# Kernel tuning notes

Hardware: AMD Instinct MI355X
Metric: run time of the kernel (lower is better)

## Reference

```python
import jax, jax.numpy as jnp
import numpy as np

MAX_DISP = 48
PATCH = 3
OFFSET = 0
PAD = PATCH // 2
EPS = 1e-3


def _unfold(x, P, pad):
    # x: [B,C,H,W] -> [B,C,K2,H,W], K2 enumerated row-major over the PxP window
    B, C, H, W = x.shape
    xp = jnp.pad(x, ((0, 0), (0, 0), (pad, pad), (pad, pad)))
    return jnp.stack([xp[:, :, i:i + H, j:j + W]
                      for i in range(P) for j in range(P)], axis=2)


def _normalize(x, axes):
    # torch F.normalize: x / clamp(||x||_2, min=eps)
    n = jnp.sqrt(jnp.sum(x * x, axis=axes, keepdims=True))
    return x / jnp.maximum(n, EPS)


def setup_inputs() -> dict:
    key = jax.random.key(0)
    k1, k2, k3 = jax.random.split(key, 3)
    shp = (2, 32, 128, 416)
    return {
        "xl": jax.random.normal(k1, shp, dtype=jnp.float32),
        "xm": jax.random.normal(k2, shp, dtype=jnp.float32),
        "xr": jax.random.normal(k3, shp, dtype=jnp.float32),
    }


def reference(xl, xm, xr):
    B, C, H, W = xl.shape
    K2 = PATCH * PATCH
    scale = (C * K2) ** 0.5

    pl = _normalize(_unfold(xl, PATCH, PAD), (1, 2))  # [B,C,K2,H,W]
    pr = _normalize(_unfold(xr, PATCH, PAD), (1, 2))
    fl = _normalize(xm, (1,))                          # [B,C,H,W]

    # fl is constant over the K2 axis, so sum patches over K2 once for sim_L/sim_R
    Sl = pl.sum(axis=2)  # [B,C,H,W]
    Sr = pr.sum(axis=2)

    cL, cR, cLR = [], [], []
    for d in range(OFFSET, OFFSET + MAX_DISP):
        if d > 0:
            # shifted_l[w] = patches_l[w+d] (zero right pad); shifted_r[w] = patches_r[w-d]
            sL = jnp.einsum('bchw,bchw->bhw', fl[..., :W - d], Sl[..., d:])
            sL = jnp.pad(sL, ((0, 0), (0, 0), (0, d)))
            sR = jnp.einsum('bchw,bchw->bhw', fl[..., d:], Sr[..., :W - d])
            sR = jnp.pad(sR, ((0, 0), (0, 0), (d, 0)))
            wlr = W - 2 * d  # overlap region of the two opposite shifts
            if wlr > 0:
                sLR = jnp.einsum('bckhw,bckhw->bhw', pl[..., 2 * d:], pr[..., :wlr])
                sLR = jnp.pad(sLR, ((0, 0), (0, 0), (d, d)))
            else:
                sLR = jnp.zeros((B, H, W), xl.dtype)
        else:
            sL = jnp.einsum('bchw,bchw->bhw', fl, Sl)
            sR = jnp.einsum('bchw,bchw->bhw', fl, Sr)
            sLR = jnp.einsum('bckhw,bckhw->bhw', pl, pr)
        cL.append(sL / scale)
        cR.append(sR / scale)
        cLR.append(sLR / scale)

    cost = jnp.stack([jnp.stack(cL, 1), jnp.stack(cR, 1), jnp.stack(cLR, 1)], axis=1)
    return jnp.clip(cost, -10.0, 10.0).astype(jnp.float16)  # [B,3,D,H,W]
```

## Files before the change

kernel.cpp:

```cpp
#include <hip/hip_runtime.h>
#include <math.h>

#define B 2
#define C 32
#define H 128
#define W 416
#define D 48
#define HW (H*W)
#define CHW (C*HW)
#define EPSN 1e-3f
#define ISCALE 0.05892556509887896f
#define LSTR 36
#define DSPL (D / 2)
#define DHALF (DSPL / 2)
#define SWZ(v) (((v) >> 1) & 7)

__device__ __forceinline__ float clip10(float x) {
    return fminf(fmaxf(x, -10.0f), 10.0f);
}

__global__ __launch_bounds__(256) void k_norm(const float* __restrict__ sql,
                                              const float* __restrict__ sqr,
                                              float* __restrict__ inl,
                                              float* __restrict__ inr) {
    int idx = blockIdx.x * 256 + threadIdx.x;
    if (idx >= B * HW) return;
    int b = idx / HW, hw = idx - b * HW;
    int h = hw / W, w = hw - h * W;
    float sl = 0.f, sr = 0.f;
#pragma unroll
    for (int di = -1; di <= 1; ++di) {
        int hh = h + di;
        if (hh < 0 || hh >= H) continue;
#pragma unroll
        for (int dj = -1; dj <= 1; ++dj) {
            int ww = w + dj;
            if (ww < 0 || ww >= W) continue;
            int p = b * HW + hh * W + ww;
            sl += sql[p];
            sr += sqr[p];
        }
    }
    inl[idx] = 1.0f / fmaxf(sqrtf(sl), EPSN);
    inr[idx] = 1.0f / fmaxf(sqrtf(sr), EPSN);
}

__device__ __forceinline__ void stage_row_v2(const float* __restrict__ gsrc,
                                             float* __restrict__ lds,
                                             int tid, int nthreads) {
    for (int t = tid; t < (W / 4) * C; t += nthreads) {
        int rw = t & 7;
        int cl = (t >> 3) & 7;
        int g  = t >> 6;
        int wg = g % 13;
        int ch = g / 13;
        int c  = ch * 8 + cl;
        int w4 = (wg * 8 + rw) * 4;
        float4 v = *(const float4*)(gsrc + (size_t)c * HW + w4);
        lds[(w4 + 0) * LSTR + c] = v.x;
        lds[(w4 + 1) * LSTR + c] = v.y;
        lds[(w4 + 2) * LSTR + c] = v.z;
        lds[(w4 + 3) * LSTR + c] = v.w;
    }
}

__device__ __forceinline__ void stage_row3_swz(const float* __restrict__ gsrc,
                                               float* __restrict__ lds,
                                               int h, int tid, int nthreads) {
    for (int t = tid; t < (W / 4) * C; t += nthreads) {
        int rw = t & 7;
        int cl = (t >> 3) & 7;
        int g  = t >> 6;
        int wg = g % 13;
        int ch = g / 13;
        int c  = ch * 8 + cl;
        int w4 = (wg * 8 + rw) * 4;
        const float* p = gsrc + (size_t)c * HW + w4;
        float4 v = *(const float4*)(p);
        if (h > 0) {
            float4 a = *(const float4*)(p - W);
            v.x += a.x; v.y += a.y; v.z += a.z; v.w += a.w;
        }
        if (h < H - 1) {
            float4 a = *(const float4*)(p + W);
            v.x += a.x; v.y += a.y; v.z += a.z; v.w += a.w;
        }
        int g2 = c >> 2, wd = c & 3;
        int sA = SWZ(w4);
        int sB_ = (sA + 1) & 7;
        lds[(w4 + 0) * LSTR + 4 * (g2 ^ sA) + wd] = v.x;
        lds[(w4 + 1) * LSTR + 4 * (g2 ^ sA) + wd] = v.y;
        lds[(w4 + 2) * LSTR + 4 * (g2 ^ sB_) + wd] = v.z;
        lds[(w4 + 3) * LSTR + 4 * (g2 ^ sB_) + wd] = v.w;
    }
}

__device__ __forceinline__ float dot32(const float* __restrict__ fl,
                                       const float* __restrict__ col) {
    const float4* c4 = (const float4*)col;
    float a = 0.0f;
#pragma unroll
    for (int q = 0; q < 8; ++q) {
        float4 v = c4[q];
        a += fl[4 * q + 0] * v.x + fl[4 * q + 1] * v.y
           + fl[4 * q + 2] * v.z + fl[4 * q + 3] * v.w;
    }
    return a;
}

__device__ __forceinline__ void dot32x2s(const float* __restrict__ fl0,
                                         const float* __restrict__ fl1,
                                         const float* __restrict__ col, int s,
                                         float& a0, float& a1) {
    const float4* c4 = (const float4*)col;
    float s0 = 0.f, s1 = 0.f;
#pragma unroll
    for (int q = 0; q < 8; ++q) {
        float4 v = c4[q ^ s];
        s0 += fl0[4 * q + 0] * v.x + fl0[4 * q + 1] * v.y
            + fl0[4 * q + 2] * v.z + fl0[4 * q + 3] * v.w;
        s1 += fl1[4 * q + 0] * v.x + fl1[4 * q + 1] * v.y
            + fl1[4 * q + 2] * v.z + fl1[4 * q + 3] * v.w;
    }
    a0 = s0; a1 = s1;
}

__global__ __launch_bounds__(448) void k_lr(const float* __restrict__ xm,
                                            const float* __restrict__ xl,
                                            const float* __restrict__ xr,
                                            const float* __restrict__ inl,
                                            const float* __restrict__ inr,
                                            float* __restrict__ out) {
    __shared__ float sB[W * LSTR];
    __shared__ float sIn[W];
    int tid = threadIdx.x;
    int h = blockIdx.x;
    int b = blockIdx.y;
    int d0 = blockIdx.z * DSPL;
    bool act = tid < W;
    int p = tid >> 1;
    int half = tid & 1;
    int w = 2 * p;
    int dbase = d0 + half * DHALF;
    int bhw = b * HW + h * W;
    const float* pm = xm + (size_t)b * CHW + h * W;

    float fl0[C], fl1[C];
    if (act) {
        float am0 = 0.f, am1 = 0.f;
#pragma unroll
        for (int c = 0; c < C; ++c) {
            float2 mv = *(const float2*)(pm + c * HW + w);
            fl0[c] = mv.x; fl1[c] = mv.y;
            am0 += mv.x * mv.x; am1 += mv.y * mv.y;
        }
        float im0 = 1.0f / fmaxf(sqrtf(am0), EPSN);
        float im1 = 1.0f / fmaxf(sqrtf(am1), EPSN);
#pragma unroll
        for (int c = 0; c < C; ++c) { fl0[c] *= im0; fl1[c] *= im1; }
    } else {
#pragma unroll
        for (int c = 0; c < C; ++c) { fl0[c] = 0.f; fl1[c] = 0.f; }
    }

    stage_row3_swz(xl + (size_t)b * CHW + h * W, sB, h, tid, 448);
    for (int j = tid; j < W; j += 448) sIn[j] = inl[bhw + j];
    __syncthreads();
    if (act) {
        float* o = out + ((size_t)b * 3 + 0) * D * HW + h * W;
        float g0a = 0.f, g0b = 0.f, g1a = 0.f, g1b = 0.f, s0p = 0.f;
#pragma unroll 3
        for (int j = 0; j <= DHALF + 2; ++j) {
            int v = w + dbase - 1 + j;
            float c0 = 0.f, c1 = 0.f;
            if (v >= 0 && v < W) dot32x2s(fl0, fl1, sB + v * LSTR, SWZ(v), c0, c1);
            float s0 = 0.f, s1 = 0.f;
            if (j >= 2) {
                int m = v - 1;
                if (m < W) {
                    float sc = sIn[m] * ISCALE;
                    s0 = clip10((g0a + g0b + c0) * sc);
                    s1 = clip10((g1a + g1b + c1) * sc);
                }
                if (j >= 3) {
                    int d = dbase + j - 3;
                    *(float2*)(o + (size_t)d * HW + w) = make_float2(s0p, s1);
                }
            }
            s0p = s0;
            g0a = g0b; g0b = c0;
            g1a = g1b; g1b = c1;
        }
    }
    __syncthreads();

    stage_row3_swz(xr + (size_t)b * CHW + h * W, sB, h, tid, 448);
    for (int j = tid; j < W; j += 448) sIn[j] = inr[bhw + j];
    __syncthreads();
    if (act) {
        float* o = out + ((size_t)b * 3 + 1) * D * HW + h * W;
        float g0a = 0.f, g0b = 0.f, g1a = 0.f, g1b = 0.f, s0p = 0.f;
#pragma unroll 3
        for (int j = 0; j <= DHALF + 2; ++j) {
            int v = w - dbase - DHALF + j;
            float c0 = 0.f, c1 = 0.f;
            if (v >= 0 && v < W) dot32x2s(fl0, fl1, sB + v * LSTR, SWZ(v), c0, c1);
            float s0 = 0.f, s1 = 0.f;
            if (j >= 2) {
                int m = v - 1;
                if (m >= 0) {
                    float sc = sIn[m] * ISCALE;
                    s0 = clip10((g0a + g0b + c0) * sc);
                    s1 = clip10((g1a + g1b + c1) * sc);
                }
                if (j >= 3) {
                    int d = dbase + DHALF + 2 - j;
                    *(float2*)(o + (size_t)d * HW + w) = make_float2(s0p, s1);
                }
            }
            s0p = s0;
            g0a = g0b; g0b = c0;
            g1a = g1b; g1b = c1;
        }
    }
}

__global__ __launch_bounds__(896) void k_e(const float* __restrict__ xl,
                                           const float* __restrict__ xr,
                                           float* __restrict__ EH,
                                           float* __restrict__ sql,
                                           float* __restrict__ sqr) {
    __shared__ float sXL[W * LSTR];
    int tid = threadIdx.x;
    int h = blockIdx.x;
    int b = blockIdx.y;
    int d0 = blockIdx.z * DSPL;
    int lane = tid & 63;
    int wv = tid >> 6;
    int half = (wv >= 7) ? 1 : 0;
    int wv7 = wv - 7 * half;
    int v = wv7 * 62 + lane - 1;
    bool vin = (v >= 0) && (v < W);
    const float* br = xr + (size_t)b * CHW + h * W;

    float xrv[C];
#pragma unroll
    for (int c = 0; c < C; ++c) xrv[c] = vin ? br[c * HW + v] : 0.0f;

    stage_row_v2(xl + (size_t)b * CHW + h * W, sXL, tid, 896);
    __syncthreads();

    bool wr = (lane >= 1) && (lane <= 62) && (v < W);

    if (blockIdx.z == 0 && half == 0) {
        float sr_ = 0.f, sl_ = 0.f;
#pragma unroll
        for (int c = 0; c < C; ++c) sr_ += xrv[c] * xrv[c];
        if (vin) {
            const float4* c4 = (const float4*)(sXL + v * LSTR);
#pragma unroll
            for (int q = 0; q < 8; ++q) {
                float4 x = c4[q];
                sl_ += x.x * x.x + x.y * x.y + x.z * x.z + x.w * x.w;
            }
        }
        if (wr) {
            sqr[b * HW + h * W + v] = sr_;
            sql[b * HW + h * W + v] = sl_;
        }
    }

    float* pe = EH + (((size_t)b * D) * H + h) * W + v;
    int dlo = d0 + half * DHALF;
    for (int d = dlo; d < dlo + DHALF; ++d) {
        int s = 2 * d;
        float e = 0.0f;
        if (vin && v + s < W) e = dot32(xrv, sXL + (v + s) * LSTR);
        float em = __shfl_up(e, 1);
        float ep = __shfl_down(e, 1);
        float eh = em + e + ep;
        if (wr) pe[(size_t)d * HW] = eh;
    }
}

#define DCH 12
__global__ __launch_bounds__(448) void k_lr2(const float* __restrict__ EH,
                                             const float* __restrict__ inl,
                                             const float* __restrict__ inr,
                                             float* __restrict__ out) {
    int w = threadIdx.x;
    int dc = blockIdx.x;
    int h = blockIdx.y;
    int b = blockIdx.z;
    if (w >= W) return;
    int bhw = b * HW + h * W;
    bool hm = (h > 0), hp = (h < H - 1);

    float* o = out + ((size_t)b * 3 + 2) * D * HW + h * W + w;
#pragma unroll
    for (int i = 0; i < DCH; ++i) {
        int d = dc * DCH + i;
        float r = 0.0f;
        if (w >= d && w + d < W) {
            int vc = w - d;
            const float* base = EH + ((size_t)b * D + d) * HW + vc;
            float e = base[h * W];
            if (hm) e += base[(h - 1) * W];
            if (hp) e += base[(h + 1) * W];
            float nl = inl[bhw + w + d];
            float nr = inr[bhw + vc];
            r = clip10(e * nl * nr * ISCALE);
        }
        o[(size_t)d * HW] = r;
    }
}

extern "C" void kernel_launch(void* const* d_in, const int* in_sizes, int n_in,
                              void* d_out, int out_size, void* d_ws, size_t ws_size,
                              hipStream_t stream) {
    const float* xl = (const float*)d_in[0];
    const float* xm = (const float*)d_in[1];
    const float* xr = (const float*)d_in[2];
    float* out = (float*)d_out;

    float* ws = (float*)d_ws;
    float* inl = ws;
    float* inr = inl + B * HW;
    float* sql = inr + B * HW;
    float* sqr = sql + B * HW;
    float* EH  = sqr + B * HW;

    k_e<<<dim3(H, B, 2), dim3(896), 0, stream>>>(xl, xr, EH, sql, sqr);
    k_norm<<<dim3((B * HW + 255) / 256), dim3(256), 0, stream>>>(sql, sqr, inl, inr);
    k_lr<<<dim3(H, B, 2), dim3(448), 0, stream>>>(xm, xl, xr, inl, inr, out);
    k_lr2<<<dim3(4, H, B), dim3(448), 0, stream>>>(EH, inl, inr, out);
}
```

Baseline: 183.1 us.

## Split k_lr over width chunks with windowed LDS staging; shrink k_e blocks

k_lr now splits each row into two width chunks of 208 columns and stages only the needed 240-column window of 3-row-summed features into LDS. This cuts shared memory per block and allows more resident blocks. Each thread pair now loads half of the xm channels and exchanges the rest via xor shuffles, and the LDS swizzle is recomputed relative to the window. k_e drops from 896 threads per block (each block covering both disparity halves) to 448 threads looping over all 24 disparities. That trades per-block parallelism for less duplicated xr loading and more blocks per CU.

```diff
diff --git a/kernel.cpp b/kernel.cpp
--- a/kernel.cpp
+++ b/kernel.cpp
@@ -13,7 +13,9 @@
 #define LSTR 36
 #define DSPL (D / 2)
 #define DHALF (DSPL / 2)
-#define SWZ(v) (((v) >> 1) & 7)
+#define WCH 208
+#define NQ 60
+#define NCOLA (NQ * 4)
 
 __device__ __forceinline__ float clip10(float x) {
     return fminf(fmaxf(x, -10.0f), 10.0f);
@@ -64,34 +66,50 @@
     }
 }
 
-__device__ __forceinline__ void stage_row3_swz(const float* __restrict__ gsrc,
-                                               float* __restrict__ lds,
-                                               int h, int tid, int nthreads) {
-    for (int t = tid; t < (W / 4) * C; t += nthreads) {
-        int rw = t & 7;
-        int cl = (t >> 3) & 7;
-        int g  = t >> 6;
-        int wg = g % 13;
-        int ch = g / 13;
-        int c  = ch * 8 + cl;
-        int w4 = (wg * 8 + rw) * 4;
-        const float* p = gsrc + (size_t)c * HW + w4;
-        float4 v = *(const float4*)(p);
-        if (h > 0) {
-            float4 a = *(const float4*)(p - W);
-            v.x += a.x; v.y += a.y; v.z += a.z; v.w += a.w;
-        }
-        if (h < H - 1) {
-            float4 a = *(const float4*)(p + W);
-            v.x += a.x; v.y += a.y; v.z += a.z; v.w += a.w;
-        }
+__device__ __forceinline__ void stage_win3(const float* __restrict__ gsrc,
+                                           float* __restrict__ lds,
+                                           int h, int v4, int tid, int nthreads) {
+    for (int t = tid; t < NQ * C; t += nthreads) {
+        int q4 = t % NQ;
+        int c  = t / NQ;
+        int idx0 = 4 * q4;
+        int v0 = v4 + idx0;
+        int s = (q4 >> 1) & 7;
         int g2 = c >> 2, wd = c & 3;
-        int sA = SWZ(w4);
-        int sB_ = (sA + 1) & 7;
-        lds[(w4 + 0) * LSTR + 4 * (g2 ^ sA) + wd] = v.x;
-        lds[(w4 + 1) * LSTR + 4 * (g2 ^ sA) + wd] = v.y;
-        lds[(w4 + 2) * LSTR + 4 * (g2 ^ sB_) + wd] = v.z;
-        lds[(w4 + 3) * LSTR + 4 * (g2 ^ sB_) + wd] = v.w;
+        float* dst = lds + (size_t)idx0 * LSTR + 4 * (g2 ^ s) + wd;
+        float4 val;
+        if (v0 >= 0 && v0 + 3 < W) {
+            const float* p = gsrc + (size_t)c * HW + v0;
+            float4 v = *(const float4*)(p);
+            if (h > 0) {
+                float4 a = *(const float4*)(p - W);
+                v.x += a.x; v.y += a.y; v.z += a.z; v.w += a.w;
+            }
+            if (h < H - 1) {
+                float4 a = *(const float4*)(p + W);
+                v.x += a.x; v.y += a.y; v.z += a.z; v.w += a.w;
+            }
+            val = v;
+        } else {
+            float e[4];
+#pragma unroll
+            for (int k = 0; k < 4; ++k) {
+                int v = v0 + k;
+                float x = 0.f;
+                if (v >= 0 && v < W) {
+                    const float* p = gsrc + (size_t)c * HW + v;
+                    x = p[0];
+                    if (h > 0) x += p[-W];
+                    if (h < H - 1) x += p[W];
+                }
+                e[k] = x;
+            }
+            val = make_float4(e[0], e[1], e[2], e[3]);
+        }
+        dst[0 * LSTR] = val.x;
+        dst[1 * LSTR] = val.y;
+        dst[2 * LSTR] = val.z;
+        dst[3 * LSTR] = val.w;
     }
 }
 
@@ -125,22 +143,25 @@
     a0 = s0; a1 = s1;
 }
 
-__global__ __launch_bounds__(448) void k_lr(const float* __restrict__ xm,
+__global__ __launch_bounds__(256) void k_lr(const float* __restrict__ xm,
                                             const float* __restrict__ xl,
                                             const float* __restrict__ xr,
                                             const float* __restrict__ inl,
                                             const float* __restrict__ inr,
                                             float* __restrict__ out) {
-    __shared__ float sB[W * LSTR];
-    __shared__ float sIn[W];
+    __shared__ float sB[NCOLA * LSTR];
+    __shared__ float sIn[NCOLA];
     int tid = threadIdx.x;
     int h = blockIdx.x;
     int b = blockIdx.y;
-    int d0 = blockIdx.z * DSPL;
-    bool act = tid < W;
+    int zd = blockIdx.z & 1;
+    int wc = blockIdx.z >> 1;
+    int d0 = zd * DSPL;
+    int w0 = wc * WCH;
+    bool act = tid < WCH;
     int p = tid >> 1;
     int half = tid & 1;
-    int w = 2 * p;
+    int w = w0 + 2 * p;
     int dbase = d0 + half * DHALF;
     int bhw = b * HW + h * W;
     const float* pm = xm + (size_t)b * CHW + h * W;
@@ -149,22 +170,30 @@
     if (act) {
         float am0 = 0.f, am1 = 0.f;
 #pragma unroll
-        for (int c = 0; c < C; ++c) {
-            float2 mv = *(const float2*)(pm + c * HW + w);
-            fl0[c] = mv.x; fl1[c] = mv.y;
+        for (int k = 0; k < 16; ++k) {
+            float2 mv = *(const float2*)(pm + (size_t)(16 * half + k) * HW + w);
+            fl0[k] = mv.x; fl1[k] = mv.y;
             am0 += mv.x * mv.x; am1 += mv.y * mv.y;
+        }
+        am0 += __shfl_xor(am0, 1);
+        am1 += __shfl_xor(am1, 1);
+#pragma unroll
+        for (int k = 0; k < 16; ++k) {
+            fl0[16 + k] = __shfl_xor(fl0[k], 1);
+            fl1[16 + k] = __shfl_xor(fl1[k], 1);
         }
         float im0 = 1.0f / fmaxf(sqrtf(am0), EPSN);
         float im1 = 1.0f / fmaxf(sqrtf(am1), EPSN);
 #pragma unroll
         for (int c = 0; c < C; ++c) { fl0[c] *= im0; fl1[c] *= im1; }
-    } else {
-#pragma unroll
-        for (int c = 0; c < C; ++c) { fl0[c] = 0.f; fl1[c] = 0.f; }
-    }
-
-    stage_row3_swz(xl + (size_t)b * CHW + h * W, sB, h, tid, 448);
-    for (int j = tid; j < W; j += 448) sIn[j] = inl[bhw + j];
+    }
+
+    int v4L = (w0 + d0 - 1) & ~3;
+    stage_win3(xl + (size_t)b * CHW + h * W, sB, h, v4L, tid, 256);
+    for (int t = tid; t < NCOLA; t += 256) {
+        int v = v4L + t;
+        sIn[t] = (v >= 0 && v < W) ? inl[bhw + v] : 0.f;
+    }
     __syncthreads();
     if (act) {
         float* o = out + ((size_t)b * 3 + 0) * D * HW + h * W;
@@ -173,12 +202,16 @@
         for (int j = 0; j <= DHALF + 2; ++j) {
             int v = w + dbase - 1 + j;
             float c0 = 0.f, c1 = 0.f;
-            if (v >= 0 && v < W) dot32x2s(fl0, fl1, sB + v * LSTR, SWZ(v), c0, c1);
+            if (v >= 0 && v < W) {
+                int idx = v - v4L;
+                int s = ((idx >> 3) & 7) ^ (half << 2);
+                dot32x2s(fl0, fl1, sB + idx * LSTR, s, c0, c1);
+            }
             float s0 = 0.f, s1 = 0.f;
             if (j >= 2) {
                 int m = v - 1;
                 if (m < W) {
-                    float sc = sIn[m] * ISCALE;
+                    float sc = sIn[m - v4L] * ISCALE;
                     s0 = clip10((g0a + g0b + c0) * sc);
                     s1 = clip10((g1a + g1b + c1) * sc);
                 }
@@ -194,8 +227,12 @@
     }
     __syncthreads();
 
-    stage_row3_swz(xr + (size_t)b * CHW + h * W, sB, h, tid, 448);
-    for (int j = tid; j < W; j += 448) sIn[j] = inr[bhw + j];
+    int v4R = (w0 - d0 - DSPL) & ~3;
+    stage_win3(xr + (size_t)b * CHW + h * W, sB, h, v4R, tid, 256);
+    for (int t = tid; t < NCOLA; t += 256) {
+        int v = v4R + t;
+        sIn[t] = (v >= 0 && v < W) ? inr[bhw + v] : 0.f;
+    }
     __syncthreads();
     if (act) {
         float* o = out + ((size_t)b * 3 + 1) * D * HW + h * W;
@@ -204,12 +241,16 @@
         for (int j = 0; j <= DHALF + 2; ++j) {
             int v = w - dbase - DHALF + j;
             float c0 = 0.f, c1 = 0.f;
-            if (v >= 0 && v < W) dot32x2s(fl0, fl1, sB + v * LSTR, SWZ(v), c0, c1);
+            if (v >= 0 && v < W) {
+                int idx = v - v4R;
+                int s = ((idx >> 3) & 7) ^ (half << 2);
+                dot32x2s(fl0, fl1, sB + idx * LSTR, s, c0, c1);
+            }
             float s0 = 0.f, s1 = 0.f;
             if (j >= 2) {
                 int m = v - 1;
                 if (m >= 0) {
-                    float sc = sIn[m] * ISCALE;
+                    float sc = sIn[m - v4R] * ISCALE;
                     s0 = clip10((g0a + g0b + c0) * sc);
                     s1 = clip10((g1a + g1b + c1) * sc);
                 }
@@ -225,7 +266,7 @@
     }
 }
 
-__global__ __launch_bounds__(896) void k_e(const float* __restrict__ xl,
+__global__ __launch_bounds__(448) void k_e(const float* __restrict__ xl,
                                            const float* __restrict__ xr,
                                            float* __restrict__ EH,
                                            float* __restrict__ sql,
@@ -237,9 +278,7 @@
     int d0 = blockIdx.z * DSPL;
     int lane = tid & 63;
     int wv = tid >> 6;
-    int half = (wv >= 7) ? 1 : 0;
-    int wv7 = wv - 7 * half;
-    int v = wv7 * 62 + lane - 1;
+    int v = wv * 62 + lane - 1;
     bool vin = (v >= 0) && (v < W);
     const float* br = xr + (size_t)b * CHW + h * W;
 
@@ -247,12 +286,12 @@
 #pragma unroll
     for (int c = 0; c < C; ++c) xrv[c] = vin ? br[c * HW + v] : 0.0f;
 
-    stage_row_v2(xl + (size_t)b * CHW + h * W, sXL, tid, 896);
+    stage_row_v2(xl + (size_t)b * CHW + h * W, sXL, tid, 448);
     __syncthreads();
 
     bool wr = (lane >= 1) && (lane <= 62) && (v < W);
 
-    if (blockIdx.z == 0 && half == 0) {
+    if (blockIdx.z == 0) {
         float sr_ = 0.f, sl_ = 0.f;
 #pragma unroll
         for (int c = 0; c < C; ++c) sr_ += xrv[c] * xrv[c];
@@ -271,8 +310,7 @@
     }
 
     float* pe = EH + (((size_t)b * D) * H + h) * W + v;
-    int dlo = d0 + half * DHALF;
-    for (int d = dlo; d < dlo + DHALF; ++d) {
+    for (int d = d0; d < d0 + DSPL; ++d) {
         int s = 2 * d;
         float e = 0.0f;
         if (vin && v + s < W) e = dot32(xrv, sXL + (v + s) * LSTR);
@@ -330,8 +368,8 @@
     float* sqr = sql + B * HW;
     float* EH  = sqr + B * HW;
 
-    k_e<<<dim3(H, B, 2), dim3(896), 0, stream>>>(xl, xr, EH, sql, sqr);
+    k_e<<<dim3(H, B, 2), dim3(448), 0, stream>>>(xl, xr, EH, sql, sqr);
     k_norm<<<dim3((B * HW + 255) / 256), dim3(256), 0, stream>>>(sql, sqr, inl, inr);
-    k_lr<<<dim3(H, B, 2), dim3(448), 0, stream>>>(xm, xl, xr, inl, inr, out);
+    k_lr<<<dim3(H, B, 4), dim3(256), 0, stream>>>(xm, xl, xr, inl, inr, out);
     k_lr2<<<dim3(4, H, B), dim3(448), 0, stream>>>(EH, inl, inr, out);
 }
```

Measured after the change: 185.3 us. Within noise of the previous version (+1.2%).
